# Performance work log

Hardware: AMD Instinct MI355X
Metric: run time of the kernel (lower is better)

## Reference

```python
import jax, jax.numpy as jnp
import numpy as np

# Human3.6M 17-joint skeleton: parent[k] is the parent joint of child joint k+1
H36M_PARENT = np.array([0, 1, 2, 0, 4, 5, 0, 7, 8, 9, 8, 11, 12, 8, 14, 15], dtype=np.int32)
EPS = 1e-12  # matches torch F.normalize default eps


def setup_inputs() -> dict:
    key = jax.random.key(0)
    B, N, J = 128, 4096, 17
    pose_3d = jax.random.normal(key, (B, N, J, 3), dtype=jnp.float32)
    return {"pose_3d": pose_3d}


def reference(pose_3d):
    # pose_3d: (B, N, J, 3).  Children are joints 1..J-1; parents given by the tree.
    parent = jnp.asarray(H36M_PARENT)
    child = pose_3d[:, :, 1:, :]                 # (B, N, K, 3)
    par = pose_3d[:, :, parent, :]               # (B, N, K, 3) single gather for all bones
    bone_vec = child - par
    bone_len = jnp.linalg.norm(bone_vec, axis=-1, keepdims=True)   # (B, N, K, 1)
    bone_dir = bone_vec / jnp.maximum(bone_len, EPS)               # F.normalize semantics
    return bone_len, bone_dir
```

## Files before the change

### kernel.cpp

```cpp
#include <hip/hip_runtime.h>
#include <math.h>


#define NJOINT 17
#define NBONE  16
#define PARENT_PACK 0xFE8CB89870540210ull

__global__ __launch_bounds__(256) void pose_bones_kernel(
    const float* __restrict__ in,
    float* __restrict__ out_len,
    float* __restrict__ out_dir,
    unsigned int total)
{
    unsigned int gid = blockIdx.x * 256u + threadIdx.x;
    if (gid >= total) return;

    const unsigned int j    = gid & 15u;
    const unsigned int pose = gid >> 4;
    const unsigned int base = pose * (NJOINT * 3u);

    const unsigned int parent = (unsigned int)((PARENT_PACK >> (4u * j)) & 15ull);

    const unsigned int coff = base + (j + 1u) * 3u;
    const unsigned int poff = base + parent * 3u;

    const float cx = in[coff + 0u];
    const float cy = in[coff + 1u];
    const float cz = in[coff + 2u];
    const float px = in[poff + 0u];
    const float py = in[poff + 1u];
    const float pz = in[poff + 2u];

    const float vx = cx - px;
    const float vy = cy - py;
    const float vz = cz - pz;

    const float len = sqrtf(vx * vx + vy * vy + vz * vz);
    const float l   = fmaxf(len, 1e-12f);

    out_len[gid] = len;
    const unsigned int doff = gid * 3u;
    out_dir[doff + 0u] = vx / l;
    out_dir[doff + 1u] = vy / l;
    out_dir[doff + 2u] = vz / l;
}

extern "C" void kernel_launch(void* const* d_in, const int* in_sizes, int n_in,
                              void* d_out, int out_size, void* d_ws, size_t ws_size,
                              hipStream_t stream) {
    const float* in = (const float*)d_in[0];
    float* out = (float*)d_out;

    const unsigned int poses = (unsigned int)(in_sizes[0] / (NJOINT * 3));
    const unsigned int total = poses * NBONE;
    float* out_len = out;
    float* out_dir = out + (size_t)total;

    const unsigned int blocks = (total + 255u) / 256u;
    pose_bones_kernel<<<blocks, 256, 0, stream>>>(in, out_len, out_dir, total);
}
```

Baseline: 218.2 us.

## Stage poses through LDS with vectorized float4 loads and coalesced stores

Each block now processes 64 poses: it loads their joints into shared memory with float4 reads, computes four bones per thread, and writes lengths as float4. Directions are staged in shared memory so they can be written back with coalesced float4 stores. This replaces strided scalar global loads and stores, which waste memory bandwidth. A scalar fallback path handles the tail, and the kernel now needs extra shared memory and block-wide synchronisation.

```diff
diff --git a/kernel.cpp b/kernel.cpp
--- a/kernel.cpp
+++ b/kernel.cpp
@@ -6,43 +6,88 @@
 #define NBONE  16
 #define PARENT_PACK 0xFE8CB89870540210ull
 
+#define PPB 64
+#define IN_FLOATS  (PPB * NJOINT * 3)
+#define DIR_FLOATS (PPB * NBONE * 3)
+#define LEN_FLOATS (PPB * NBONE)
+
 __global__ __launch_bounds__(256) void pose_bones_kernel(
     const float* __restrict__ in,
     float* __restrict__ out_len,
     float* __restrict__ out_dir,
-    unsigned int total)
+    unsigned int P)
 {
-    unsigned int gid = blockIdx.x * 256u + threadIdx.x;
-    if (gid >= total) return;
+    __shared__ float s_in[IN_FLOATS];
+    __shared__ float s_dir[DIR_FLOATS];
 
-    const unsigned int j    = gid & 15u;
-    const unsigned int pose = gid >> 4;
-    const unsigned int base = pose * (NJOINT * 3u);
+    const unsigned int tid   = threadIdx.x;
+    const unsigned int block = blockIdx.x;
+    const unsigned int pose0 = block * PPB;
 
-    const unsigned int parent = (unsigned int)((PARENT_PACK >> (4u * j)) & 15ull);
+    if (pose0 + PPB <= P) {
+        const float4* gin  = (const float4*)(in + (size_t)pose0 * (NJOINT * 3));
+        float4*       sin4 = (float4*)s_in;
+        sin4[tid]       = gin[tid];
+        sin4[tid + 256] = gin[tid + 256];
+        sin4[tid + 512] = gin[tid + 512];
+        if (tid < IN_FLOATS / 4 - 768) sin4[tid + 768] = gin[tid + 768];
+        __syncthreads();
 
-    const unsigned int coff = base + (j + 1u) * 3u;
-    const unsigned int poff = base + parent * 3u;
+        const unsigned int p  = tid >> 2;
+        const unsigned int j0 = (tid & 3u) * 4u;
+        const float* pp = s_in + p * (NJOINT * 3);
 
-    const float cx = in[coff + 0u];
-    const float cy = in[coff + 1u];
-    const float cz = in[coff + 2u];
-    const float px = in[poff + 0u];
-    const float py = in[poff + 1u];
-    const float pz = in[poff + 2u];
+        float lenv[4];
+        float dirv[12];
+        #pragma unroll
+        for (int i = 0; i < 4; ++i) {
+            const unsigned int j = j0 + (unsigned int)i;
+            const unsigned int parent = (unsigned int)((PARENT_PACK >> (4u * j)) & 15ull);
+            const float vx = pp[(j + 1u) * 3u + 0u] - pp[parent * 3u + 0u];
+            const float vy = pp[(j + 1u) * 3u + 1u] - pp[parent * 3u + 1u];
+            const float vz = pp[(j + 1u) * 3u + 2u] - pp[parent * 3u + 2u];
+            const float len = sqrtf(vx * vx + vy * vy + vz * vz);
+            const float l   = fmaxf(len, 1e-12f);
+            lenv[i] = len;
+            dirv[i * 3 + 0] = vx / l;
+            dirv[i * 3 + 1] = vy / l;
+            dirv[i * 3 + 2] = vz / l;
+        }
 
-    const float vx = cx - px;
-    const float vy = cy - py;
-    const float vz = cz - pz;
+        ((float4*)(out_len + (size_t)pose0 * NBONE))[tid] =
+            make_float4(lenv[0], lenv[1], lenv[2], lenv[3]);
 
-    const float len = sqrtf(vx * vx + vy * vy + vz * vz);
-    const float l   = fmaxf(len, 1e-12f);
+        float4* sd4 = (float4*)(s_dir + tid * 12u);
+        sd4[0] = make_float4(dirv[0], dirv[1], dirv[2],  dirv[3]);
+        sd4[1] = make_float4(dirv[4], dirv[5], dirv[6],  dirv[7]);
+        sd4[2] = make_float4(dirv[8], dirv[9], dirv[10], dirv[11]);
+        __syncthreads();
 
-    out_len[gid] = len;
-    const unsigned int doff = gid * 3u;
-    out_dir[doff + 0u] = vx / l;
-    out_dir[doff + 1u] = vy / l;
-    out_dir[doff + 2u] = vz / l;
+        float4*       gdir = (float4*)(out_dir + (size_t)pose0 * (NBONE * 3));
+        const float4* sd   = (const float4*)s_dir;
+        gdir[tid]       = sd[tid];
+        gdir[tid + 256] = sd[tid + 256];
+        gdir[tid + 512] = sd[tid + 512];
+    } else {
+        const unsigned int total = P * NBONE;
+        for (unsigned int gid = pose0 * NBONE + tid; gid < total; gid += 256u) {
+            const unsigned int j    = gid & 15u;
+            const unsigned int pose = gid >> 4;
+            const unsigned int base = pose * (NJOINT * 3u);
+            const unsigned int parent = (unsigned int)((PARENT_PACK >> (4u * j)) & 15ull);
+            const unsigned int coff = base + (j + 1u) * 3u;
+            const unsigned int poff = base + parent * 3u;
+            const float vx = in[coff + 0u] - in[poff + 0u];
+            const float vy = in[coff + 1u] - in[poff + 1u];
+            const float vz = in[coff + 2u] - in[poff + 2u];
+            const float len = sqrtf(vx * vx + vy * vy + vz * vz);
+            const float l   = fmaxf(len, 1e-12f);
+            out_len[gid] = len;
+            out_dir[gid * 3u + 0u] = vx / l;
+            out_dir[gid * 3u + 1u] = vy / l;
+            out_dir[gid * 3u + 2u] = vz / l;
+        }
+    }
 }
 
 extern "C" void kernel_launch(void* const* d_in, const int* in_sizes, int n_in,
@@ -51,11 +96,10 @@
     const float* in = (const float*)d_in[0];
     float* out = (float*)d_out;
 
-    const unsigned int poses = (unsigned int)(in_sizes[0] / (NJOINT * 3));
-    const unsigned int total = poses * NBONE;
+    const unsigned int P = (unsigned int)(in_sizes[0] / (NJOINT * 3));
     float* out_len = out;
-    float* out_dir = out + (size_t)total;
+    float* out_dir = out + (size_t)P * NBONE;
 
-    const unsigned int blocks = (total + 255u) / 256u;
-    pose_bones_kernel<<<blocks, 256, 0, stream>>>(in, out_len, out_dir, total);
+    const unsigned int blocks = (P + PPB - 1u) / PPB;
+    pose_bones_kernel<<<blocks, 256, 0, stream>>>(in, out_len, out_dir, P);
 }
```

New measurement: 211.4 us. 3.1% less time.
